# Optimization experiments

Measured on AMD Instinct MI355X. Metric: run time of the kernel, lower is better.

## Reference

```python
import jax, jax.numpy as jnp
import numpy as np

NUM_CLIPS = 64
# (kernel, stride) per layer for each scale, per num_scale_layers=[16,8,8]
SCALE_SPECS = [[(1, 1)] + [(2, 1)] * 15,
               [(3, 2)] + [(2, 1)] * 7,
               [(3, 2)] + [(2, 1)] * 7]
KEEP = {0: (7, 15), 1: (3, 7), 2: (3, 5, 7)}


def _build_props():
    # replicates SparsePropMaxPool.__init__ construction of self.props
    tmp = [[1] * 16, [2] + [1] * 7, [2] + [1] * 7]
    acum, stride, props = 0, 1, []
    for scale_idx, strides in enumerate(tmp):
        for i, st in enumerate(strides):
            stride *= st
            if i in KEEP[scale_idx]:
                s = np.arange(0, NUM_CLIPS - acum - i * stride, stride)
                props.append(np.stack([s, s + acum + i * stride], -1))
        acum += stride * (len(strides) + 1)
    props = np.concatenate(props, 0)
    props[:, 1] += 1
    return props.astype(np.int64)  # [153, 2]


def _maxpool1d(x, k, s):
    if k == 1 and s == 1:
        return x
    return jax.lax.reduce_window(x, -jnp.inf, jax.lax.max,
                                 (1, 1, k), (1, 1, s), 'VALID')


def _forward(x, props):
    B, H, N = x.shape  # N == 64
    acum, stride = 0, 1
    s_parts, e_parts, feat_parts = [], [], []
    for scale in SCALE_SPECS:
        for i, (k, st) in enumerate(scale):
            stride *= st
            x = _maxpool1d(x, k, st)
            s = np.arange(0, N - acum - i * stride, stride)
            s_parts.append(s)
            e_parts.append(s + acum + i * stride)
            feat_parts.append(x)  # [B, H, len(s)]
        acum += stride * (len(scale) + 1)
    # all (s,e) diagonals are disjoint across layers -> one fused scatter
    s_all = np.concatenate(s_parts)
    e_all = np.concatenate(e_parts)
    feats = jnp.concatenate(feat_parts, axis=-1)  # [B, H, total]
    ori_map_h = jnp.zeros((B, H, N, N), x.dtype).at[:, :, s_all, e_all].set(feats)
    ori_map_mask = jnp.zeros((B, 1, N, N), x.dtype).at[:, :, s_all, e_all].set(1.0)
    p0, p1 = props[:, 0], props[:, 1] - 1
    props_h = jnp.transpose(ori_map_h[:, :, p0, p1], (0, 2, 1))  # [B, P, H]
    # faithful (no-op) write-back as in the torch source
    ori_map_h = ori_map_h.at[:, :, p0, p1].set(jnp.transpose(props_h, (0, 2, 1)))
    return props_h, ori_map_h, ori_map_mask


def setup_inputs() -> dict:
    key = jax.random.key(0)
    kx, kg = jax.random.split(key)
    x = jax.random.normal(kx, (64, 512, 64), dtype=jnp.float32)
    props = jnp.asarray(_build_props())  # [153, 2]
    props_graph = jax.random.randint(kg, (153, 153), 0, 2, dtype=jnp.int32)
    return {'x': x, 'props': props, 'props_graph': props_graph}


def reference(x, props, props_graph):
    return _forward(x, props)
```

## Files before the change

kernel.cpp:

```cpp
#include <hip/hip_runtime.h>


#define B_ 64
#define H_ 512
#define N_ 64
#define NPROP 153

__device__ __forceinline__ bool in_set(int s, int d) {
    if (d < 0) return false;
    if (d <= 15) return true;
    if (d <= 31) return (d & 1) && ((s & 1) == 0);
    return (d >= 35) && ((d & 3) == 3) && ((s & 3) == 0);
}

__global__ __launch_bounds__(128) void fused_kernel(const float* __restrict__ x,
                                                    float* __restrict__ out_props,
                                                    float* __restrict__ out_map,
                                                    float* __restrict__ out_mask) {
    const int lane = threadIdx.x;
    const int bid  = blockIdx.x;

    if ((bid & 7) == 0) {
        const int b  = bid >> 6;
        const int m  = (bid >> 3) & 7;
        const int h  = m * 64 + (lane & 63);
        const int q  = lane >> 6;

        const float4* xr = reinterpret_cast<const float4*>(x + ((size_t)b * H_ + h) * N_);
        float r[64];
        #pragma unroll
        for (int k = 0; k < 16; ++k) {
            float4 v = xr[k];
            r[4*k+0] = v.x; r[4*k+1] = v.y; r[4*k+2] = v.z; r[4*k+3] = v.w;
        }
        float a[63];
        #pragma unroll
        for (int i = 0; i < 63; ++i) a[i] = fmaxf(r[i], r[i+1]);
        float bb[61];
        #pragma unroll
        for (int i = 0; i < 61; ++i) bb[i] = fmaxf(a[i], a[i+2]);
        float T3[57];
        #pragma unroll
        for (int i = 0; i < 57; ++i) T3[i] = fmaxf(bb[i], bb[i+4]);

        float* po = out_props + (size_t)b * NPROP * H_ + h;
        if (q == 0) {
            #pragma unroll
            for (int s = 0; s < 57; ++s)
                po[(size_t)s * H_] = T3[s];
            #pragma unroll
            for (int s = 0; s < 20; ++s)
                po[(size_t)(57 + s) * H_] = fmaxf(T3[s], T3[s + 8]);
        } else {
            #pragma unroll
            for (int s = 20; s < 49; ++s)
                po[(size_t)(57 + s) * H_] = fmaxf(T3[s], T3[s + 8]);
            int p = 106;
            #pragma unroll
            for (int s = 0; s <= 40; s += 2)
                po[(size_t)(p++) * H_] = fmaxf(fmaxf(T3[s], T3[s + 8]), T3[s + 16]);
            #pragma unroll
            for (int s = 0; s <= 32; s += 2)
                po[(size_t)(p++) * H_] =
                    fmaxf(fmaxf(T3[s], T3[s + 8]), fmaxf(T3[s + 16], T3[s + 24]));
            #pragma unroll
            for (int s = 0; s <= 16; s += 4) {
                float mx = T3[s];
                #pragma unroll
                for (int j = 8; j <= 40; j += 8) mx = fmaxf(mx, T3[s + j]);
                po[(size_t)(p++) * H_] = mx;
            }
            #pragma unroll
            for (int s = 0; s <= 8; s += 4) {
                float mx = T3[s];
                #pragma unroll
                for (int j = 8; j <= 48; j += 8) mx = fmaxf(mx, T3[s + j]);
                po[(size_t)(p++) * H_] = mx;
            }
            {
                float mx = T3[0];
                #pragma unroll
                for (int j = 8; j <= 56; j += 8) mx = fmaxf(mx, T3[j]);
                po[(size_t)p * H_] = mx;
            }
        }

        if (m == 0) {
            float* mk = out_mask + (size_t)b * (N_ * N_);
            const int e = lane & 63;
            #pragma unroll
            for (int i = 0; i < 32; ++i) {
                int s = 2 * i + q;
                mk[s * N_ + e] = in_set(s, e - s) ? 1.0f : 0.0f;
            }
        }
    }

    const int g = lane >> 4;
    const int t = lane & 15;
    const size_t bh = (size_t)bid * 8 + g;

    __shared__ __align__(16) float xs[8][72];
    float4 xv = reinterpret_cast<const float4*>(x)[bid * 128 + lane];
    *reinterpret_cast<float4*>(&xs[g][4 * t]) = xv;
    __syncthreads();

    float4* mrow = reinterpret_cast<float4*>(out_map + bh * (size_t)(N_ * N_));
    const int e0 = 4 * t;
    float vx = 0.f, vy = 0.f, vz = 0.f, vw = 0.f;
    #pragma unroll
    for (int s = N_ - 1; s >= 0; --s) {
        const float mv = xs[g][s];
        vx = (s == e0 + 0) ? mv : fmaxf(vx, mv);
        vy = (s == e0 + 1) ? mv : fmaxf(vy, mv);
        vz = (s == e0 + 2) ? mv : fmaxf(vz, mv);
        vw = (s == e0 + 3) ? mv : fmaxf(vw, mv);
        float4 w;
        w.x = in_set(s, e0 + 0 - s) ? vx : 0.f;
        w.y = in_set(s, e0 + 1 - s) ? vy : 0.f;
        w.z = in_set(s, e0 + 2 - s) ? vz : 0.f;
        w.w = in_set(s, e0 + 3 - s) ? vw : 0.f;
        mrow[s * 16 + t] = w;
    }
}

extern "C" void kernel_launch(void* const* d_in, const int* in_sizes, int n_in,
                              void* d_out, int out_size, void* d_ws, size_t ws_size,
                              hipStream_t stream) {
    const float* x = (const float*)d_in[0];
    float* out       = (float*)d_out;
    float* out_props = out;
    float* out_map   = out + (size_t)B_ * NPROP * H_;
    float* out_mask  = out_map + (size_t)B_ * H_ * N_ * N_;

    fused_kernel<<<dim3(B_ * H_ / 8), dim3(128), 0, stream>>>(x, out_props, out_map, out_mask);
}
```

Baseline: 120.7 us.

## Spread props computation across all blocks via shared-memory T3 rows

```diff
diff --git a/kernel.cpp b/kernel.cpp
--- a/kernel.cpp
+++ b/kernel.cpp
@@ -5,6 +5,7 @@
 #define H_ 512
 #define N_ 64
 #define NPROP 153
+#define T3PITCH 65
 
 __device__ __forceinline__ bool in_set(int s, int d) {
     if (d < 0) return false;
@@ -13,114 +14,92 @@
     return (d >= 35) && ((d & 3) == 3) && ((s & 3) == 0);
 }
 
+__device__ __forceinline__ void decode_prop(int p, int& s, int& nw) {
+    if (p < 57)       { s = p;           nw = 1; }
+    else if (p < 106) { s = p - 57;      nw = 2; }
+    else if (p < 127) { s = 2*(p - 106); nw = 3; }
+    else if (p < 144) { s = 2*(p - 127); nw = 4; }
+    else if (p < 149) { s = 4*(p - 144); nw = 6; }
+    else if (p < 152) { s = 4*(p - 149); nw = 7; }
+    else              { s = 0;           nw = 8; }
+}
+
 __global__ __launch_bounds__(128) void fused_kernel(const float* __restrict__ x,
                                                     float* __restrict__ out_props,
                                                     float* __restrict__ out_map,
                                                     float* __restrict__ out_mask) {
-    const int lane = threadIdx.x;
-    const int bid  = blockIdx.x;
+    const int tid = threadIdx.x;
+    const int bid = blockIdx.x;
+    const int g   = tid >> 4;
+    const int t   = tid & 15;
 
-    if ((bid & 7) == 0) {
-        const int b  = bid >> 6;
-        const int m  = (bid >> 3) & 7;
-        const int h  = m * 64 + (lane & 63);
-        const int q  = lane >> 6;
+    __shared__ __align__(16) float xs[8][72];
+    __shared__ float T3s[8][T3PITCH];
 
-        const float4* xr = reinterpret_cast<const float4*>(x + ((size_t)b * H_ + h) * N_);
-        float r[64];
-        #pragma unroll
-        for (int k = 0; k < 16; ++k) {
-            float4 v = xr[k];
-            r[4*k+0] = v.x; r[4*k+1] = v.y; r[4*k+2] = v.z; r[4*k+3] = v.w;
-        }
-        float a[63];
-        #pragma unroll
-        for (int i = 0; i < 63; ++i) a[i] = fmaxf(r[i], r[i+1]);
-        float bb[61];
-        #pragma unroll
-        for (int i = 0; i < 61; ++i) bb[i] = fmaxf(a[i], a[i+2]);
-        float T3[57];
-        #pragma unroll
-        for (int i = 0; i < 57; ++i) T3[i] = fmaxf(bb[i], bb[i+4]);
+    float4 xv = reinterpret_cast<const float4*>(x)[bid * 128 + tid];
+    *reinterpret_cast<float4*>(&xs[g][4 * t]) = xv;
+    __syncthreads();
 
-        float* po = out_props + (size_t)b * NPROP * H_ + h;
-        if (q == 0) {
+    {
+        const int i  = tid & 63;
+        const int g2 = tid >> 6;
+        if (i < 57) {
             #pragma unroll
-            for (int s = 0; s < 57; ++s)
-                po[(size_t)s * H_] = T3[s];
-            #pragma unroll
-            for (int s = 0; s < 20; ++s)
-                po[(size_t)(57 + s) * H_] = fmaxf(T3[s], T3[s + 8]);
-        } else {
-            #pragma unroll
-            for (int s = 20; s < 49; ++s)
-                po[(size_t)(57 + s) * H_] = fmaxf(T3[s], T3[s + 8]);
-            int p = 106;
-            #pragma unroll
-            for (int s = 0; s <= 40; s += 2)
-                po[(size_t)(p++) * H_] = fmaxf(fmaxf(T3[s], T3[s + 8]), T3[s + 16]);
-            #pragma unroll
-            for (int s = 0; s <= 32; s += 2)
-                po[(size_t)(p++) * H_] =
-                    fmaxf(fmaxf(T3[s], T3[s + 8]), fmaxf(T3[s + 16], T3[s + 24]));
-            #pragma unroll
-            for (int s = 0; s <= 16; s += 4) {
-                float mx = T3[s];
+            for (int it = 0; it < 4; ++it) {
+                const int row = it * 2 + g2;
+                float m = xs[row][i];
                 #pragma unroll
-                for (int j = 8; j <= 40; j += 8) mx = fmaxf(mx, T3[s + j]);
-                po[(size_t)(p++) * H_] = mx;
-            }
-            #pragma unroll
-            for (int s = 0; s <= 8; s += 4) {
-                float mx = T3[s];
-                #pragma unroll
-                for (int j = 8; j <= 48; j += 8) mx = fmaxf(mx, T3[s + j]);
-                po[(size_t)(p++) * H_] = mx;
-            }
-            {
-                float mx = T3[0];
-                #pragma unroll
-                for (int j = 8; j <= 56; j += 8) mx = fmaxf(mx, T3[j]);
-                po[(size_t)p * H_] = mx;
-            }
-        }
-
-        if (m == 0) {
-            float* mk = out_mask + (size_t)b * (N_ * N_);
-            const int e = lane & 63;
-            #pragma unroll
-            for (int i = 0; i < 32; ++i) {
-                int s = 2 * i + q;
-                mk[s * N_ + e] = in_set(s, e - s) ? 1.0f : 0.0f;
+                for (int j = 1; j < 8; ++j) m = fmaxf(m, xs[row][i + j]);
+                T3s[row][i] = m;
             }
         }
     }
 
-    const int g = lane >> 4;
-    const int t = lane & 15;
-    const size_t bh = (size_t)bid * 8 + g;
+    {
+        const size_t bh = (size_t)bid * 8 + g;
+        float4* mrow = reinterpret_cast<float4*>(out_map + bh * (size_t)(N_ * N_));
+        const int e0 = 4 * t;
+        float vx = 0.f, vy = 0.f, vz = 0.f, vw = 0.f;
+        #pragma unroll
+        for (int s = N_ - 1; s >= 0; --s) {
+            const float mv = xs[g][s];
+            vx = (s == e0 + 0) ? mv : fmaxf(vx, mv);
+            vy = (s == e0 + 1) ? mv : fmaxf(vy, mv);
+            vz = (s == e0 + 2) ? mv : fmaxf(vz, mv);
+            vw = (s == e0 + 3) ? mv : fmaxf(vw, mv);
+            float4 w;
+            w.x = in_set(s, e0 + 0 - s) ? vx : 0.f;
+            w.y = in_set(s, e0 + 1 - s) ? vy : 0.f;
+            w.z = in_set(s, e0 + 2 - s) ? vz : 0.f;
+            w.w = in_set(s, e0 + 3 - s) ? vw : 0.f;
+            mrow[s * 16 + t] = w;
+        }
+    }
 
-    __shared__ __align__(16) float xs[8][72];
-    float4 xv = reinterpret_cast<const float4*>(x)[bid * 128 + lane];
-    *reinterpret_cast<float4*>(&xs[g][4 * t]) = xv;
     __syncthreads();
 
-    float4* mrow = reinterpret_cast<float4*>(out_map + bh * (size_t)(N_ * N_));
-    const int e0 = 4 * t;
-    float vx = 0.f, vy = 0.f, vz = 0.f, vw = 0.f;
-    #pragma unroll
-    for (int s = N_ - 1; s >= 0; --s) {
-        const float mv = xs[g][s];
-        vx = (s == e0 + 0) ? mv : fmaxf(vx, mv);
-        vy = (s == e0 + 1) ? mv : fmaxf(vy, mv);
-        vz = (s == e0 + 2) ? mv : fmaxf(vz, mv);
-        vw = (s == e0 + 3) ? mv : fmaxf(vw, mv);
-        float4 w;
-        w.x = in_set(s, e0 + 0 - s) ? vx : 0.f;
-        w.y = in_set(s, e0 + 1 - s) ? vy : 0.f;
-        w.z = in_set(s, e0 + 2 - s) ? vz : 0.f;
-        w.w = in_set(s, e0 + 3 - s) ? vw : 0.f;
-        mrow[s * 16 + t] = w;
+    {
+        const int b  = bid >> 6;
+        const int h0 = (bid & 63) * 8;
+        float* po = out_props + (size_t)b * NPROP * H_ + h0;
+        #pragma unroll
+        for (int k = tid; k < NPROP * 8; k += 128) {
+            const int p = k >> 3, hoff = k & 7;
+            int s, nw; decode_prop(p, s, nw);
+            float m = T3s[hoff][s];
+            for (int j = 1; j < nw; ++j) m = fmaxf(m, T3s[hoff][s + 8 * j]);
+            po[(size_t)p * H_ + hoff] = m;
+        }
+    }
+
+    if ((bid & 63) == 0) {
+        float* mk = out_mask + (size_t)(bid >> 6) * (N_ * N_);
+        #pragma unroll
+        for (int i = 0; i < 32; ++i) {
+            const int idx = tid + i * 128;
+            const int s = idx >> 6, e = idx & 63;
+            mk[idx] = in_set(s, e - s) ? 1.0f : 0.0f;
+        }
     }
 }
 
```

Result: slower. 133.1 us (+10.3%).
